# Optimization experiments

Hardware: AMD Instinct MI355X
Metric: run time of the kernel (lower is better)

## Reference

```python
import jax, jax.numpy as jnp
import numpy as np

B, S, D, QD, OUT = 32, 2048, 768, 256, 1024

def setup_inputs() -> dict:
    key = jax.random.key(0)
    k = jax.random.split(key, 8)
    data = jax.random.normal(k[0], (B, S, D), dtype=jnp.float32)
    seq_len = jax.random.randint(k[1], (B,), 0, S)
    # learned params (Linear: y = x @ W.T + b)
    s1 = 1.0 / np.sqrt(D)
    s3 = 1.0 / np.sqrt(QD)
    W1 = jax.random.uniform(k[2], (QD, D), minval=-s1, maxval=s1, dtype=jnp.float32)
    b1 = jax.random.uniform(k[3], (QD,), minval=-s1, maxval=s1, dtype=jnp.float32)
    W2 = jax.random.uniform(k[4], (QD, D), minval=-s1, maxval=s1, dtype=jnp.float32)
    b2 = jax.random.uniform(k[5], (QD,), minval=-s1, maxval=s1, dtype=jnp.float32)
    W3 = jax.random.uniform(k[6], (OUT, QD), minval=-s3, maxval=s3, dtype=jnp.float32)
    b3 = jax.random.uniform(k[7], (OUT,), minval=-s3, maxval=s3, dtype=jnp.float32)
    return {"data": data, "seq_len": seq_len, "W1": W1, "b1": b1,
            "W2": W2, "b2": b2, "W3": W3, "b3": b3}

def reference(data, seq_len, W1, b1, W2, b2, W3, b3):
    # Q, K projections: [B,S,QD]
    Q = jnp.einsum('bsd,qd->bsq', data, W1) + b1
    K = jnp.einsum('bsd,qd->bsq', data, W2) + b2
    # scores = K @ Q^T / sqrt(QD): [B,S,S]
    scores = jnp.einsum('biq,bjq->bij', K, Q) / np.sqrt(QD).astype(np.float32)
    attn = jax.nn.softmax(scores, axis=2)
    # attention output uses K as values: [B,S,QD]
    x = jnp.einsum('bij,bjq->biq', attn, K)
    # max-pool over sequence dim -> [B,QD]
    x = jnp.max(x, axis=1)
    out = jax.nn.relu(jnp.einsum('bq,oq->bo', x, W3) + b3)
    return out
```

## Files before the change

### kernel.cpp

```cpp
#include <hip/hip_runtime.h>
#include <hip/hip_bf16.h>

#define Bn   32
#define Sn   2048
#define Dn   768
#define QDn  256
#define OUTn 1024

typedef __attribute__((ext_vector_type(8))) short          bf16x8;
typedef __attribute__((ext_vector_type(4))) float          f32x4;
typedef __attribute__((ext_vector_type(8))) unsigned short u16x8;
typedef __attribute__((ext_vector_type(4))) unsigned short u16x4;

typedef unsigned short ushort_t;

__device__ __forceinline__ unsigned short f2bf(float f) {
    unsigned int u = __float_as_uint(f);
    u = (u + 0x7FFFu + ((u >> 16) & 1u)) >> 16;
    return (unsigned short)u;
}
#define MFMA16(a,b,c) __builtin_amdgcn_mfma_f32_16x16x32_bf16((a),(b),(c),0,0,0)

__global__ __launch_bounds__(256) void wconv_kernel(
    const float* __restrict__ W1, const float* __restrict__ W2,
    ushort_t* __restrict__ W1h, ushort_t* __restrict__ W2h)
{
    const int idx = blockIdx.x * 256 + threadIdx.x;
    W1h[idx] = f2bf(W1[idx]);
    W2h[idx] = f2bf(W2[idx]);
}

__global__ __launch_bounds__(256, 2) void proj_kernel(
    const float* __restrict__ data,
    const ushort_t* __restrict__ W1h, const float* __restrict__ b1,
    const ushort_t* __restrict__ W2h, const float* __restrict__ b2,
    ushort_t* __restrict__ Qb, ushort_t* __restrict__ Kb,
    ushort_t* __restrict__ KTb)
{
    __shared__ __align__(16) char smem[34816];
    ushort_t* DH = (ushort_t*)smem;
    ushort_t* WH = (ushort_t*)(smem + 10240);
    ushort_t* EP = (ushort_t*)smem;

    const int tid  = threadIdx.x;
    const int w    = tid >> 6;
    const int quad = (tid >> 4) & 3;
    const int n15  = tid & 15;
    const int mtile = blockIdx.y;
    const int half  = blockIdx.x;
    const bool isQ  = (half == 0);
    const ushort_t* WhP = isQ ? W1h : W2h;
    const float* bp = isQ ? b1 : b2;

    f32x4 acc[2][16];
    #pragma unroll
    for (int i = 0; i < 2; ++i)
        #pragma unroll
        for (int j = 0; j < 16; ++j) acc[i][j] = (f32x4)0.f;

    const size_t drow = (size_t)mtile * 128;

    for (int kt = 0; kt < 24; ++kt) {
        const int kc = kt * 32;
        {
            const int m  = tid >> 1;
            const int k0 = (tid & 1) << 4;
            const float* src = data + (drow + m) * 768 + kc + k0;
            const float4 v0 = *(const float4*)(src);
            const float4 v1 = *(const float4*)(src + 4);
            const float4 v2 = *(const float4*)(src + 8);
            const float4 v3 = *(const float4*)(src + 12);
            u16x8 h0, h1;
            h0[0]=f2bf(v0.x); h0[1]=f2bf(v0.y); h0[2]=f2bf(v0.z); h0[3]=f2bf(v0.w);
            h0[4]=f2bf(v1.x); h0[5]=f2bf(v1.y); h0[6]=f2bf(v1.z); h0[7]=f2bf(v1.w);
            h1[0]=f2bf(v2.x); h1[1]=f2bf(v2.y); h1[2]=f2bf(v2.z); h1[3]=f2bf(v2.w);
            h1[4]=f2bf(v3.x); h1[5]=f2bf(v3.y); h1[6]=f2bf(v3.z); h1[7]=f2bf(v3.w);
            *(u16x8*)&DH[m*40 + k0]     = h0;
            *(u16x8*)&DH[m*40 + k0 + 8] = h1;
        }
        #pragma unroll
        for (int u = 0; u < 4; ++u) {
            const int nrow = (tid >> 2) + u * 64;
            const int ko   = (tid & 3) << 3;
            *(u16x8*)&WH[nrow*40 + ko] = *(const u16x8*)(WhP + (size_t)nrow * 768 + kc + ko);
        }
        __syncthreads();
        bf16x8 ah[2];
        #pragma unroll
        for (int ms = 0; ms < 2; ++ms)
            ah[ms] = *(bf16x8*)&DH[(w*32 + ms*16 + n15)*40 + quad*8];
        #pragma unroll
        for (int ns = 0; ns < 16; ++ns) {
            const bf16x8 bh = *(bf16x8*)&WH[(ns*16 + n15)*40 + quad*8];
            #pragma unroll
            for (int ms = 0; ms < 2; ++ms)
                acc[ms][ns] = MFMA16(ah[ms], bh, acc[ms][ns]);
        }
        __syncthreads();
    }

    float bv[16];
    #pragma unroll
    for (int ns = 0; ns < 16; ++ns) bv[ns] = bp[ns*16 + n15];

    {
        ushort_t* dstRM = isQ ? Qb : Kb;
        #pragma unroll
        for (int hf = 0; hf < 2; ++hf) {
            __syncthreads();
            if ((w >> 1) == hf) {
                #pragma unroll
                for (int ms = 0; ms < 2; ++ms)
                    #pragma unroll
                    for (int ns = 0; ns < 16; ++ns)
                        #pragma unroll
                        for (int r = 0; r < 4; ++r) {
                            const int rl = (w & 1)*32 + ms*16 + quad*4 + r;
                            EP[rl*264 + ns*16 + n15] = f2bf(acc[ms][ns][r] + bv[ns]);
                        }
            }
            __syncthreads();
            const int row = tid >> 2;
            #pragma unroll
            for (int u = 0; u < 8; ++u) {
                const int co = (tid & 3)*8 + u*32;
                *(u16x8*)(dstRM + (drow + hf*64 + row)*256 + co) =
                    *(u16x8*)&EP[row*264 + co];
            }
        }
    }
    if (!isQ) {
        const int bidx = mtile >> 4;
        const int s0   = (mtile & 15) * 128;
        #pragma unroll
        for (int qh = 0; qh < 2; ++qh) {
            __syncthreads();
            #pragma unroll
            for (int ms = 0; ms < 2; ++ms)
                #pragma unroll
                for (int ns8 = 0; ns8 < 8; ++ns8) {
                    const int ns = qh*8 + ns8;
                    #pragma unroll
                    for (int r = 0; r < 4; ++r) {
                        const int rowm = w*32 + ms*16 + quad*4 + r;
                        EP[(ns8*16 + n15)*136 + rowm] = f2bf(acc[ms][ns][r] + bv[ns]);
                    }
                }
            __syncthreads();
            const int q = tid >> 1;
            #pragma unroll
            for (int u = 0; u < 8; ++u) {
                const int mo = (tid & 1)*8 + u*16;
                *(u16x8*)(KTb + ((size_t)(bidx*256 + qh*128 + q))*2048 + s0 + mo) =
                    *(u16x8*)&EP[q*136 + mo];
            }
        }
    }
}

__global__ __launch_bounds__(256, 2) void attn_kernel(
    const ushort_t* __restrict__ Qb, const ushort_t* __restrict__ Kb,
    const ushort_t* __restrict__ KTb, float* __restrict__ pmax)
{
    __shared__ __align__(16) char smem[49664];
    ushort_t* QS = (ushort_t*)smem;
    ushort_t* PS = (ushort_t*)(smem + 32768);
    float*    l_lds = (float*)(smem + 49152);

    const int tid  = threadIdx.x;
    const int w    = tid >> 6;
    const int quad = (tid >> 4) & 3;
    const int n15  = tid & 15;
    const int b    = blockIdx.x;
    const int it   = blockIdx.y;
    const int i0   = it * 128;

    const ushort_t* QbB  = Qb  + (size_t)b * Sn * QDn;
    const ushort_t* KbB  = Kb  + (size_t)b * Sn * QDn;
    const ushort_t* KTbB = KTb + (size_t)b * QDn * Sn;

    bf16x8 kf[2][8];
    #pragma unroll
    for (int isub = 0; isub < 2; ++isub) {
        const size_t irow = (size_t)(i0 + w*32 + isub*16 + n15) * QDn;
        #pragma unroll
        for (int ks = 0; ks < 8; ++ks)
            kf[isub][ks] = *(const bf16x8*)(KbB + irow + ks*32 + quad*8);
    }

    f32x4 xq[4][8];
    #pragma unroll
    for (int qs = 0; qs < 4; ++qs)
        #pragma unroll
        for (int is = 0; is < 8; ++is) xq[qs][is] = (f32x4)0.f;
    float l_i[2] = {0.f, 0.f};

    const int swz  = (n15 & 7) * 8;
    const int jrow = tid >> 2;
    const int wsw  = (jrow & 7) * 8;

    for (int jt = 0; jt < Sn; jt += 64) {
        __syncthreads();
        {
            const ushort_t* src = QbB + (size_t)(jt + jrow) * QDn + (tid & 3) * 64;
            ushort_t* dst = QS + jrow * 256;
            #pragma unroll
            for (int u = 0; u < 8; ++u) {
                const int col = (tid & 3) * 64 + u * 8;
                *(u16x8*)&dst[col ^ wsw] = *(const u16x8*)(src + u * 8);
            }
        }
        __syncthreads();
        f32x4 sc[4][2];
        #pragma unroll
        for (int js = 0; js < 4; ++js) { sc[js][0] = (f32x4)0.f; sc[js][1] = (f32x4)0.f; }
        #pragma unroll
        for (int ks = 0; ks < 8; ++ks) {
            #pragma unroll
            for (int js = 0; js < 4; ++js) {
                const bf16x8 ah = *(bf16x8*)&QS[(js*16 + n15)*256 + ((ks*32 + quad*8) ^ swz)];
                sc[js][0] = MFMA16(ah, kf[0][ks], sc[js][0]);
                sc[js][1] = MFMA16(ah, kf[1][ks], sc[js][1]);
            }
        }
        #pragma unroll
        for (int isub = 0; isub < 2; ++isub) {
            const int prow = (w*32 + isub*16 + n15) * 64;
            float rs = 0.f;
            #pragma unroll
            for (int js = 0; js < 4; ++js) {
                u16x4 ph;
                #pragma unroll
                for (int r = 0; r < 4; ++r) {
                    const float p = __expf(sc[js][isub][r] * 0.0625f);
                    rs += p;
                    ph[r] = f2bf(p);
                }
                *(u16x4*)&PS[prow + ((js*16 + quad*4) ^ swz)] = ph;
            }
            rs += __shfl_xor(rs, 16, 64);
            rs += __shfl_xor(rs, 32, 64);
            l_i[isub] += rs;
        }
        bf16x8 at2[2][4];
        #pragma unroll
        for (int ks2 = 0; ks2 < 2; ++ks2)
            #pragma unroll
            for (int qs = 0; qs < 4; ++qs)
                at2[ks2][qs] = *(const bf16x8*)(
                    KTbB + (size_t)(w*64 + qs*16 + n15) * Sn + jt + ks2*32 + quad*8);
        __syncthreads();
        #pragma unroll
        for (int ks2 = 0; ks2 < 2; ++ks2) {
            #pragma unroll
            for (int is = 0; is < 8; ++is) {
                const bf16x8 pb = *(bf16x8*)&PS[(is*16 + n15)*64 + ((ks2*32 + quad*8) ^ swz)];
                #pragma unroll
                for (int qs = 0; qs < 4; ++qs)
                    xq[qs][is] = MFMA16(at2[ks2][qs], pb, xq[qs][is]);
            }
        }
    }

    __syncthreads();
    if (quad == 0) {
        l_lds[w*32 + n15]      = l_i[0];
        l_lds[w*32 + 16 + n15] = l_i[1];
    }
    __syncthreads();
    float linv[8];
    #pragma unroll
    for (int is = 0; is < 8; ++is) linv[is] = 1.0f / l_lds[is*16 + n15];
    #pragma unroll
    for (int qs = 0; qs < 4; ++qs) {
        #pragma unroll
        for (int r = 0; r < 4; ++r) {
            float mv = xq[qs][0][r] * linv[0];
            #pragma unroll
            for (int is = 1; is < 8; ++is)
                mv = fmaxf(mv, xq[qs][is][r] * linv[is]);
            mv = fmaxf(mv, __shfl_xor(mv, 1, 64));
            mv = fmaxf(mv, __shfl_xor(mv, 2, 64));
            mv = fmaxf(mv, __shfl_xor(mv, 4, 64));
            mv = fmaxf(mv, __shfl_xor(mv, 8, 64));
            if (n15 == 0) {
                const int q = w*64 + qs*16 + quad*4 + r;
                pmax[((size_t)b * 16 + it) * QDn + q] = mv;
            }
        }
    }
}

__global__ __launch_bounds__(256) void head_kernel(
    const float* __restrict__ pmax,
    const float* __restrict__ W3, const float* __restrict__ b3,
    float* __restrict__ out)
{
    __shared__ float xs[QDn];
    const int b = blockIdx.x, tid = threadIdx.x;
    float m = pmax[((size_t)b * 16) * QDn + tid];
    #pragma unroll
    for (int t = 1; t < 16; ++t)
        m = fmaxf(m, pmax[((size_t)b * 16 + t) * QDn + tid]);
    xs[tid] = m;
    __syncthreads();
    #pragma unroll
    for (int u = 0; u < 4; ++u) {
        const int o = (u << 8) + tid;
        const float4* wv = (const float4*)(W3 + (size_t)o * QDn);
        float s = 0.f;
        #pragma unroll 8
        for (int q4 = 0; q4 < QDn / 4; ++q4) {
            const float4 w4 = wv[q4];
            const float4 x4 = *(const float4*)&xs[q4 << 2];
            s += w4.x * x4.x + w4.y * x4.y + w4.z * x4.z + w4.w * x4.w;
        }
        out[(size_t)b * OUTn + o] = fmaxf(s + b3[o], 0.f);
    }
}

extern "C" void kernel_launch(void* const* d_in, const int* in_sizes, int n_in,
                              void* d_out, int out_size, void* d_ws, size_t ws_size,
                              hipStream_t stream) {
    const float* data = (const float*)d_in[0];
    const float* W1 = (const float*)d_in[2];
    const float* b1 = (const float*)d_in[3];
    const float* W2 = (const float*)d_in[4];
    const float* b2 = (const float*)d_in[5];
    const float* W3 = (const float*)d_in[6];
    const float* b3 = (const float*)d_in[7];
    float* out = (float*)d_out;

    ushort_t* Qb  = (ushort_t*)d_ws;
    ushort_t* Kb  = Qb  + 16777216;
    ushort_t* KTb = Kb  + 16777216;
    float*    pmax = (float*)((char*)d_ws + 100663296);
    ushort_t* W1h = (ushort_t*)((char*)d_ws + 100663296 + 524288);
    ushort_t* W2h = W1h + 196608;

    wconv_kernel<<<768, 256, 0, stream>>>(W1, W2, W1h, W2h);
    dim3 gP(2, 512);
    proj_kernel<<<gP, 256, 0, stream>>>(data, W1h, b1, W2h, b2, Qb, Kb, KTb);
    dim3 gA(Bn, 16);
    attn_kernel<<<gA, 256, 0, stream>>>(Qb, Kb, KTb, pmax);
    head_kernel<<<Bn, 256, 0, stream>>>(pmax, W3, b3, out);
}
```

Measured before the change: 663.9 us.

## Prefetch next Q tile into registers during attention and split head kernel grid

The attention loop now loads the next 64-row Q tile from global memory into registers at the start of each iteration. It writes that tile into shared memory after the score phase, so global latency overlaps the MFMA work and one barrier per iteration goes away. The K^T fragment loads are moved up into the softmax loop so they issue earlier. The head kernel is spread over a 2D grid of 32x4 blocks instead of 32 blocks, with each thread computing one output. The prefetch raises register pressure, which may lower occupancy.

```diff
diff --git a/kernel.cpp b/kernel.cpp
--- a/kernel.cpp
+++ b/kernel.cpp
@@ -179,6 +179,24 @@
     const ushort_t* KbB  = Kb  + (size_t)b * Sn * QDn;
     const ushort_t* KTbB = KTb + (size_t)b * QDn * Sn;
 
+    const int sr  = tid >> 2;
+    const int sc0 = (tid & 3) * 8;
+    const int ssw = (sr & 7) * 8;
+    const ushort_t* sQrow = QbB + (size_t)sr * QDn + sc0;
+    ushort_t* sDrow = QS + sr * 256;
+
+    f32x4 xq[4][8];
+    #pragma unroll
+    for (int qs = 0; qs < 4; ++qs)
+        #pragma unroll
+        for (int is = 0; is < 8; ++is) xq[qs][is] = (f32x4)0.f;
+    float l_i[2] = {0.f, 0.f};
+
+    u16x8 qst[8];
+    #pragma unroll
+    for (int u = 0; u < 8; ++u) qst[u] = *(const u16x8*)(sQrow + u*32);
+    #pragma unroll
+    for (int u = 0; u < 8; ++u) *(u16x8*)&sDrow[(sc0 + u*32) ^ ssw] = qst[u];
     bf16x8 kf[2][8];
     #pragma unroll
     for (int isub = 0; isub < 2; ++isub) {
@@ -187,30 +205,17 @@
         for (int ks = 0; ks < 8; ++ks)
             kf[isub][ks] = *(const bf16x8*)(KbB + irow + ks*32 + quad*8);
     }
-
-    f32x4 xq[4][8];
-    #pragma unroll
-    for (int qs = 0; qs < 4; ++qs)
-        #pragma unroll
-        for (int is = 0; is < 8; ++is) xq[qs][is] = (f32x4)0.f;
-    float l_i[2] = {0.f, 0.f};
-
-    const int swz  = (n15 & 7) * 8;
-    const int jrow = tid >> 2;
-    const int wsw  = (jrow & 7) * 8;
+    __syncthreads();
+
+    const int swz = (n15 & 7) * 8;
 
     for (int jt = 0; jt < Sn; jt += 64) {
-        __syncthreads();
-        {
-            const ushort_t* src = QbB + (size_t)(jt + jrow) * QDn + (tid & 3) * 64;
-            ushort_t* dst = QS + jrow * 256;
-            #pragma unroll
-            for (int u = 0; u < 8; ++u) {
-                const int col = (tid & 3) * 64 + u * 8;
-                *(u16x8*)&dst[col ^ wsw] = *(const u16x8*)(src + u * 8);
-            }
-        }
-        __syncthreads();
+        const bool pf = (jt + 64 < Sn);
+        if (pf) {
+            const ushort_t* src = sQrow + (size_t)(jt + 64) * QDn;
+            #pragma unroll
+            for (int u = 0; u < 8; ++u) qst[u] = *(const u16x8*)(src + u*32);
+        }
         f32x4 sc[4][2];
         #pragma unroll
         for (int js = 0; js < 4; ++js) { sc[js][0] = (f32x4)0.f; sc[js][1] = (f32x4)0.f; }
@@ -223,6 +228,7 @@
                 sc[js][1] = MFMA16(ah, kf[1][ks], sc[js][1]);
             }
         }
+        bf16x8 at2[2][4];
         #pragma unroll
         for (int isub = 0; isub < 2; ++isub) {
             const int prow = (w*32 + isub*16 + n15) * 64;
@@ -241,15 +247,21 @@
             rs += __shfl_xor(rs, 16, 64);
             rs += __shfl_xor(rs, 32, 64);
             l_i[isub] += rs;
-        }
-        bf16x8 at2[2][4];
-        #pragma unroll
-        for (int ks2 = 0; ks2 < 2; ++ks2)
-            #pragma unroll
-            for (int qs = 0; qs < 4; ++qs)
-                at2[ks2][qs] = *(const bf16x8*)(
-                    KTbB + (size_t)(w*64 + qs*16 + n15) * Sn + jt + ks2*32 + quad*8);
+            if (isub == 0) {
+                #pragma unroll
+                for (int ks2 = 0; ks2 < 2; ++ks2)
+                    #pragma unroll
+                    for (int qs = 0; qs < 4; ++qs)
+                        at2[ks2][qs] = *(const bf16x8*)(
+                            KTbB + (size_t)(w*64 + qs*16 + n15) * Sn + jt + ks2*32 + quad*8);
+            }
+        }
         __syncthreads();
+        if (pf) {
+            #pragma unroll
+            for (int u = 0; u < 8; ++u)
+                *(u16x8*)&sDrow[(sc0 + u*32) ^ ssw] = qst[u];
+        }
         #pragma unroll
         for (int ks2 = 0; ks2 < 2; ++ks2) {
             #pragma unroll
@@ -260,9 +272,9 @@
                     xq[qs][is] = MFMA16(at2[ks2][qs], pb, xq[qs][is]);
             }
         }
-    }
-
-    __syncthreads();
+        __syncthreads();
+    }
+
     if (quad == 0) {
         l_lds[w*32 + n15]      = l_i[0];
         l_lds[w*32 + 16 + n15] = l_i[1];
@@ -304,19 +316,16 @@
         m = fmaxf(m, pmax[((size_t)b * 16 + t) * QDn + tid]);
     xs[tid] = m;
     __syncthreads();
-    #pragma unroll
-    for (int u = 0; u < 4; ++u) {
-        const int o = (u << 8) + tid;
-        const float4* wv = (const float4*)(W3 + (size_t)o * QDn);
-        float s = 0.f;
-        #pragma unroll 8
-        for (int q4 = 0; q4 < QDn / 4; ++q4) {
-            const float4 w4 = wv[q4];
-            const float4 x4 = *(const float4*)&xs[q4 << 2];
-            s += w4.x * x4.x + w4.y * x4.y + w4.z * x4.z + w4.w * x4.w;
-        }
-        out[(size_t)b * OUTn + o] = fmaxf(s + b3[o], 0.f);
-    }
+    const int o = blockIdx.y * 256 + tid;
+    const float4* wv = (const float4*)(W3 + (size_t)o * QDn);
+    float s = 0.f;
+    #pragma unroll 8
+    for (int q4 = 0; q4 < QDn / 4; ++q4) {
+        const float4 w4 = wv[q4];
+        const float4 x4 = *(const float4*)&xs[q4 << 2];
+        s += w4.x * x4.x + w4.y * x4.y + w4.z * x4.z + w4.w * x4.w;
+    }
+    out[(size_t)b * OUTn + o] = fmaxf(s + b3[o], 0.f);
 }
 
 extern "C" void kernel_launch(void* const* d_in, const int* in_sizes, int n_in,
@@ -343,5 +352,6 @@
     proj_kernel<<<gP, 256, 0, stream>>>(data, W1h, b1, W2h, b2, Qb, Kb, KTb);
     dim3 gA(Bn, 16);
     attn_kernel<<<gA, 256, 0, stream>>>(Qb, Kb, KTb, pmax);
-    head_kernel<<<Bn, 256, 0, stream>>>(pmax, W3, b3, out);
-}
+    dim3 gH(Bn, 4);
+    head_kernel<<<gH, 256, 0, stream>>>(pmax, W3, b3, out);
+}
```

Result: slower. 920.3 us (+38.6%).
